# Optimization experiments

Hardware: AMD Instinct MI355X
Metric: run time of the kernel (lower is better)

Reference implementation:

```python
import jax, jax.numpy as jnp
import numpy as np

BETA = 0.99
EPS = 1e-05


def setup_inputs() -> dict:
    key = jax.random.key(0)
    s = jax.random.normal(key, (16, 2000, 257, 2), dtype=jnp.float32)
    return {"s": s}


def reference(s):
    # s: (N, T, F, C). Unbiased EWMA mean/var normalization, sequential over T.
    N, T, F, C = s.shape
    st = jnp.transpose(s, (1, 0, 2, 3))  # (T, N, F, C) for scan over time
    zeros = jnp.zeros((N, F, C), dtype=s.dtype)
    one = jnp.asarray(1.0, dtype=s.dtype)
    beta = jnp.asarray(BETA, dtype=s.dtype)

    def step(carry, x):
        beta_t, v1, v2, S = carry
        beta_t = beta * beta_t
        v1 = beta * v1 + (1 - beta) * x
        v2_prev = v2
        v2 = v1 / (1 - beta_t)
        w = (1 - beta) / (1 - beta_t)
        S = (1 - w) * S + w * (x - v2) * (x - v2_prev)
        S = S * (S > 0)  # clamp negative variance to 0 (as in original)
        y = (x - v2) / jnp.sqrt(S + EPS)
        return (beta_t, v1, v2, S), y

    init = (one, zeros, zeros, zeros)
    _, out = jax.lax.scan(step, init, st)
    return jnp.transpose(out, (1, 0, 2, 3))  # back to (N, T, F, C)
```

## Files before the change

### kernel.cpp

```cpp
#include <hip/hip_runtime.h>


#define NN 16
#define TT 2000
#define FCC 514
#define SERIES (NN * FCC)
#define BETAF 0.99f
#define OMBF 0.01f
#define EPSF 1e-5f
#define NCHUNK 7
#define CLEN 286
#define WARM 512
#define PF 16

__global__ __launch_bounds__(64)
void ewma_kernel(const float* __restrict__ s, float* __restrict__ out) {
    const int tid = blockIdx.x * 64 + threadIdx.x;
    if (tid >= SERIES) return;

    const int chunk = blockIdx.y;
    const int t_out = chunk * CLEN;
    int t_end = t_out + CLEN; if (t_end > TT) t_end = TT;
    int t0 = t_out - WARM;     if (t0 < 0) t0 = 0;

    const int n  = tid / FCC;
    const int fc = tid - n * FCC;

    double bd = 0.99, acc = 1.0;
    int e = t0;
    while (e) { if (e & 1) acc *= bd; bd *= bd; e >>= 1; }
    float bt = (float)acc;

    float v1 = 0.0f, v2p = 0.0f, S = 0.0f;

    const size_t base = (size_t)n * TT * FCC + (size_t)fc + (size_t)t0 * FCC;
    const float* p  = s   + base;
    float*       po = out + base;

    auto step = [&](float x) -> float {
        bt *= BETAF;
        const float om = 1.0f - bt;
        const float r  = __builtin_amdgcn_rcpf(om);
        v1 = fmaf(BETAF, v1 - x, x);
        const float v2 = v1 * r;
        const float w  = OMBF * r;
        const float d  = x - v2;
        const float dp = x - v2p;
        const float pr = d * dp;
        S = fmaf(w, pr - S, S);
        S = fmaxf(S, 0.0f);
        const float y = d * __builtin_amdgcn_rsqf(S + EPSF);
        v2p = v2;
        return y;
    };

    float buf[PF];
    #pragma unroll
    for (int i = 0; i < PF; ++i) buf[i] = p[i * FCC];

    int t = t0;
    while (t + PF <= t_end) {
        const float* pf_ptr = (t + 2 * PF <= t_end) ? (p + PF * FCC) : p;
        float nbuf[PF];
        #pragma unroll
        for (int i = 0; i < PF; ++i) nbuf[i] = pf_ptr[i * FCC];

        #pragma unroll
        for (int i = 0; i < PF; ++i) {
            const float y = step(buf[i]);
            if (t >= t_out) {
                po[i * FCC] = y;
            } else if (t + i >= t_out) {
                po[i * FCC] = y;
            }
        }

        #pragma unroll
        for (int i = 0; i < PF; ++i) buf[i] = nbuf[i];
        p  += PF * FCC;
        po += PF * FCC;
        t  += PF;
    }
    for (; t < t_end; ++t) {
        const float y = step(*p);
        if (t >= t_out) *po = y;
        p  += FCC;
        po += FCC;
    }
}

extern "C" void kernel_launch(void* const* d_in, const int* in_sizes, int n_in,
                              void* d_out, int out_size, void* d_ws, size_t ws_size,
                              hipStream_t stream) {
    const float* s = (const float*)d_in[0];
    float* out = (float*)d_out;
    dim3 grid((SERIES + 63) / 64, NCHUNK);
    ewma_kernel<<<grid, dim3(64), 0, stream>>>(s, out);
}
```

Measured before the change: 154.7 us.

## Precompute bias-correction table in LDS and split time into more chunks

```diff
diff --git a/kernel.cpp b/kernel.cpp
--- a/kernel.cpp
+++ b/kernel.cpp
@@ -8,28 +8,38 @@
 #define BETAF 0.99f
 #define OMBF 0.01f
 #define EPSF 1e-5f
-#define NCHUNK 7
-#define CLEN 286
+#define NCHUNK 16
+#define CLEN 125
 #define WARM 512
 #define PF 16
+#define TABMAX (WARM + CLEN)
 
 __global__ __launch_bounds__(64)
 void ewma_kernel(const float* __restrict__ s, float* __restrict__ out) {
-    const int tid = blockIdx.x * 64 + threadIdx.x;
-    if (tid >= SERIES) return;
+    __shared__ float2 tab[TABMAX];
 
     const int chunk = blockIdx.y;
     const int t_out = chunk * CLEN;
     int t_end = t_out + CLEN; if (t_end > TT) t_end = TT;
     int t0 = t_out - WARM;     if (t0 < 0) t0 = 0;
+    const int L = t_end - t0;
+
+    for (int i = threadIdx.x; i < L; i += 64) {
+        double bd = 0.99, acc = 1.0;
+        int e = t0 + i + 1;
+        #pragma unroll
+        for (int k = 0; k < 11; ++k) { if (e & 1) acc *= bd; bd *= bd; e >>= 1; }
+        const float om = 1.0f - (float)acc;
+        const float r  = __builtin_amdgcn_rcpf(om);
+        tab[i] = make_float2(r, OMBF * r);
+    }
+    __syncthreads();
+
+    const int tid = blockIdx.x * 64 + threadIdx.x;
+    if (tid >= SERIES) return;
 
     const int n  = tid / FCC;
     const int fc = tid - n * FCC;
-
-    double bd = 0.99, acc = 1.0;
-    int e = t0;
-    while (e) { if (e & 1) acc *= bd; bd *= bd; e >>= 1; }
-    float bt = (float)acc;
 
     float v1 = 0.0f, v2p = 0.0f, S = 0.0f;
 
@@ -37,17 +47,14 @@
     const float* p  = s   + base;
     float*       po = out + base;
 
-    auto step = [&](float x) -> float {
-        bt *= BETAF;
-        const float om = 1.0f - bt;
-        const float r  = __builtin_amdgcn_rcpf(om);
-        v1 = fmaf(BETAF, v1 - x, x);
-        const float v2 = v1 * r;
-        const float w  = OMBF * r;
-        const float d  = x - v2;
-        const float dp = x - v2p;
-        const float pr = d * dp;
-        S = fmaf(w, pr - S, S);
+    auto step = [&](float x, float2 rw) -> float {
+        const float r = rw.x, w = rw.y;
+        v1 = fmaf(BETAF, v1, OMBF * x);
+        const float v2  = v1 * r;
+        const float d   = x - v2;
+        const float dp  = x - v2p;
+        const float wpr = w * (d * dp);
+        S = fmaf(S, 1.0f - w, wpr);
         S = fmaxf(S, 0.0f);
         const float y = d * __builtin_amdgcn_rsqf(S + EPSF);
         v2p = v2;
@@ -59,6 +66,7 @@
     for (int i = 0; i < PF; ++i) buf[i] = p[i * FCC];
 
     int t = t0;
+    int li = 0;
     while (t + PF <= t_end) {
         const float* pf_ptr = (t + 2 * PF <= t_end) ? (p + PF * FCC) : p;
         float nbuf[PF];
@@ -67,7 +75,7 @@
 
         #pragma unroll
         for (int i = 0; i < PF; ++i) {
-            const float y = step(buf[i]);
+            const float y = step(buf[i], tab[li + i]);
             if (t >= t_out) {
                 po[i * FCC] = y;
             } else if (t + i >= t_out) {
@@ -80,9 +88,10 @@
         p  += PF * FCC;
         po += PF * FCC;
         t  += PF;
+        li += PF;
     }
-    for (; t < t_end; ++t) {
-        const float y = step(*p);
+    for (; t < t_end; ++t, ++li) {
+        const float y = step(*p, tab[li]);
         if (t >= t_out) *po = y;
         p  += FCC;
         po += FCC;
```

Measured after the change: 165.2 us. +6.8%, slower.

## Stage input through LDS with async global_load_lds triple buffering per batch row

Applied to the files above, without the earlier changes.

```diff
diff --git a/kernel.cpp b/kernel.cpp
--- a/kernel.cpp
+++ b/kernel.cpp
@@ -4,89 +4,220 @@
 #define NN 16
 #define TT 2000
 #define FCC 514
-#define SERIES (NN * FCC)
+#define BPT 2056
 #define BETAF 0.99f
 #define OMBF 0.01f
 #define EPSF 1e-5f
 #define NCHUNK 7
 #define CLEN 286
 #define WARM 512
-#define PF 16
-
-__global__ __launch_bounds__(64)
+#define G 16
+#define GRPB (G * BPT)
+#define SLOTB 36864
+#define NSLOT 3
+
+__device__ __constant__ const float BP[G + 1] = {
+    1.0f, 0.99f, 0.9801f, 0.970299f, 0.96059601f, 0.9509900499f,
+    0.941480149401f, 0.93206534790699f, 0.9227446944279201f,
+    0.9134272474836409f, 0.9042929750088045f, 0.8952500452587165f,
+    0.8862975448061293f, 0.877434569357868f, 0.8686602236642894f,
+    0.8599736214276465f, 0.8513738852133700f
+};
+
+#define READX                                                                \
+    float x[G];                                                              \
+    {                                                                        \
+        unsigned a = ldsbase + (unsigned)((g % NSLOT) * SLOTB) + d           \
+                   + (unsigned)fc * 4u;                                      \
+        _Pragma("unroll")                                                    \
+        for (int i = 0; i < G; ++i) {                                        \
+            asm volatile("ds_read_b32 %0, %1" : "=v"(x[i]) : "v"(a));        \
+            a += BPT;                                                        \
+        }                                                                    \
+        asm volatile("s_waitcnt lgkmcnt(0)" ::: "memory");                   \
+        __builtin_amdgcn_sched_barrier(0);                                   \
+    }
+
+#define RCPB                                                                 \
+    float rr[G];                                                             \
+    _Pragma("unroll")                                                        \
+    for (int i = 0; i < G; ++i)                                              \
+        rr[i] = __builtin_amdgcn_rcpf(1.0f - btg * BP[i]);                   \
+    btg *= BP[G];
+
+#define KEEP16(Y)                                                            \
+    asm volatile("" :: "v"(Y[0]), "v"(Y[1]), "v"(Y[2]), "v"(Y[3]),           \
+                       "v"(Y[4]), "v"(Y[5]), "v"(Y[6]), "v"(Y[7]),           \
+                       "v"(Y[8]), "v"(Y[9]), "v"(Y[10]), "v"(Y[11]),         \
+                       "v"(Y[12]), "v"(Y[13]), "v"(Y[14]), "v"(Y[15]));
+
+#define BODY_OUT(Y)                                                          \
+    {                                                                        \
+        READX                                                                \
+        STAGE(g + 2);                                                        \
+        RCPB                                                                 \
+        float* pg = Ofp + (size_t)t * FCC + fc;                              \
+        _Pragma("unroll")                                                    \
+        for (int i = 0; i < G; ++i) {                                        \
+            const float xx = x[i];                                           \
+            const float r  = rr[i];                                          \
+            v1 = fmaf(BETAF, v1, OMBF * xx);                                 \
+            const float v2 = v1 * r;                                         \
+            const float dd = xx - v2;                                        \
+            const float dp = xx - v2p;                                       \
+            S = fmaf(OMBF * r, dd * dp - S, S);                              \
+            S = fmaxf(S, 0.0f);                                              \
+            Y[i] = dd * __builtin_amdgcn_rsqf(S + EPSF);                     \
+            v2p = v2;                                                        \
+            if (fc < FCC)                                                    \
+                asm volatile("global_store_dword %0, %1, off"                \
+                             :: "v"(pg + i * FCC), "v"(Y[i]));               \
+        }                                                                    \
+            \
+        asm volatile("s_waitcnt vmcnt(20)" ::: "memory");                    \
+        __builtin_amdgcn_sched_barrier(0);                                   \
+        KEEP16(yA) KEEP16(yB)                                                \
+        __builtin_amdgcn_s_barrier();                                        \
+    }
+
+__global__ __launch_bounds__(576, 1)
 void ewma_kernel(const float* __restrict__ s, float* __restrict__ out) {
-    const int tid = blockIdx.x * 64 + threadIdx.x;
-    if (tid >= SERIES) return;
-
+    __shared__ char lds[NSLOT * SLOTB];
+
+    const int lane = threadIdx.x & 63;
+    const int wid  = threadIdx.x >> 6;
+    const int fc   = threadIdx.x;
+    const int n    = blockIdx.x;
     const int chunk = blockIdx.y;
+
     const int t_out = chunk * CLEN;
     int t_end = t_out + CLEN; if (t_end > TT) t_end = TT;
     int t0 = t_out - WARM;     if (t0 < 0) t0 = 0;
 
-    const int n  = tid / FCC;
-    const int fc = tid - n * FCC;
-
-    double bd = 0.99, acc = 1.0;
-    int e = t0;
-    while (e) { if (e & 1) acc *= bd; bd *= bd; e >>= 1; }
-    float bt = (float)acc;
+    const char* Bn     = (const char*)s + (size_t)n * TT * BPT;
+    const char* send16 = (const char*)s + (size_t)NN * TT * BPT - 16;
+    const unsigned d   = (unsigned)((t0 & 1) * 8);
+
+    const unsigned ldsbase =
+        (unsigned)(uintptr_t)(__attribute__((address_space(3))) char*)lds;
+
+    const char* Astage0 = Bn + (size_t)t0 * BPT - d;
+
+    auto STAGE = [&](int k) {
+        const char* A = Astage0 + (size_t)k * GRPB;
+        char* slot = lds + (k % NSLOT) * SLOTB;
+        #pragma unroll
+        for (int j = 0; j < 4; ++j) {
+            const int o = wid * 4 + j;
+            const char* src = A + o * 1024 + lane * 16;
+            if (src > send16) src = send16;
+            __builtin_amdgcn_global_load_lds(
+                (const __attribute__((address_space(1))) void*)src,
+                (__attribute__((address_space(3))) void*)(slot + o * 1024),
+                16, 0, 0);
+        }
+    };
+
+    float btg;
+    {
+        double bd = 0.99, acc = 0.99;
+        int e = t0;
+        while (e) { if (e & 1) acc *= bd; bd *= bd; e >>= 1; }
+        btg = (float)acc;
+    }
 
     float v1 = 0.0f, v2p = 0.0f, S = 0.0f;
-
-    const size_t base = (size_t)n * TT * FCC + (size_t)fc + (size_t)t0 * FCC;
-    const float* p  = s   + base;
-    float*       po = out + base;
-
-    auto step = [&](float x) -> float {
-        bt *= BETAF;
-        const float om = 1.0f - bt;
-        const float r  = __builtin_amdgcn_rcpf(om);
-        v1 = fmaf(BETAF, v1 - x, x);
-        const float v2 = v1 * r;
-        const float w  = OMBF * r;
-        const float d  = x - v2;
-        const float dp = x - v2p;
-        const float pr = d * dp;
-        S = fmaf(w, pr - S, S);
-        S = fmaxf(S, 0.0f);
-        const float y = d * __builtin_amdgcn_rsqf(S + EPSF);
-        v2p = v2;
-        return y;
-    };
-
-    float buf[PF];
+    float* Ofp = out + (size_t)n * TT * FCC;
+
+    STAGE(0); STAGE(1);
+    asm volatile("s_waitcnt vmcnt(4)" ::: "memory");
+    __builtin_amdgcn_sched_barrier(0);
+    __builtin_amdgcn_s_barrier();
+
+    int t = t0, g = 0;
+
+    while (t + G <= t_out) {
+        READX
+        STAGE(g + 2);
+        RCPB
+        #pragma unroll
+        for (int i = 0; i < G; ++i) {
+            const float xx = x[i];
+            const float r  = rr[i];
+            v1 = fmaf(BETAF, v1, OMBF * xx);
+            const float v2 = v1 * r;
+            const float dd = xx - v2;
+            const float dp = xx - v2p;
+            S = fmaf(OMBF * r, dd * dp - S, S);
+            S = fmaxf(S, 0.0f);
+            v2p = v2;
+        }
+        asm volatile("s_waitcnt vmcnt(4)" ::: "memory");
+        __builtin_amdgcn_sched_barrier(0);
+        __builtin_amdgcn_s_barrier();
+        ++g; t += G;
+    }
+
+    if (t < t_out && t + G <= t_end) {
+        READX
+        STAGE(g + 2);
+        RCPB
+        float* pg = Ofp + (size_t)t * FCC + fc;
+        #pragma unroll
+        for (int i = 0; i < G; ++i) {
+            const float xx = x[i];
+            const float r  = rr[i];
+            v1 = fmaf(BETAF, v1, OMBF * xx);
+            const float v2 = v1 * r;
+            const float dd = xx - v2;
+            const float dp = xx - v2p;
+            S = fmaf(OMBF * r, dd * dp - S, S);
+            S = fmaxf(S, 0.0f);
+            const float y = dd * __builtin_amdgcn_rsqf(S + EPSF);
+            v2p = v2;
+            if (t + i >= t_out && fc < FCC)
+                asm volatile("global_store_dword %0, %1, off"
+                             :: "v"(pg + i * FCC), "v"(y));
+        }
+        asm volatile("s_waitcnt vmcnt(0)" ::: "memory");
+        __builtin_amdgcn_sched_barrier(0);
+        __builtin_amdgcn_s_barrier();
+        ++g; t += G;
+    }
+
+    float yA[G], yB[G];
     #pragma unroll
-    for (int i = 0; i < PF; ++i) buf[i] = p[i * FCC];
-
-    int t = t0;
-    while (t + PF <= t_end) {
-        const float* pf_ptr = (t + 2 * PF <= t_end) ? (p + PF * FCC) : p;
-        float nbuf[PF];
-        #pragma unroll
-        for (int i = 0; i < PF; ++i) nbuf[i] = pf_ptr[i * FCC];
-
-        #pragma unroll
-        for (int i = 0; i < PF; ++i) {
-            const float y = step(buf[i]);
-            if (t >= t_out) {
-                po[i * FCC] = y;
-            } else if (t + i >= t_out) {
-                po[i * FCC] = y;
-            }
-        }
-
-        #pragma unroll
-        for (int i = 0; i < PF; ++i) buf[i] = nbuf[i];
-        p  += PF * FCC;
-        po += PF * FCC;
-        t  += PF;
-    }
-    for (; t < t_end; ++t) {
-        const float y = step(*p);
-        if (t >= t_out) *po = y;
-        p  += FCC;
-        po += FCC;
-    }
+    for (int i = 0; i < G; ++i) { yA[i] = 0.0f; yB[i] = 0.0f; }
+    int cur = 0;
+    while (t + G <= t_end) {
+        if (cur == 0) BODY_OUT(yA)
+        else          BODY_OUT(yB)
+        cur ^= 1;
+        ++g; t += G;
+    }
+
+    {
+        const int R = t_end - t;
+        const float* slotf = (const float*)(lds + (g % NSLOT) * SLOTB);
+        const unsigned d4 = d >> 2;
+        for (int i = 0; i < R; ++i) {
+            const float xx = slotf[d4 + i * FCC + fc];
+            const float r  = __builtin_amdgcn_rcpf(1.0f - btg);
+            btg *= BETAF;
+            v1 = fmaf(BETAF, v1, OMBF * xx);
+            const float v2 = v1 * r;
+            const float dd = xx - v2;
+            const float dp = xx - v2p;
+            S = fmaf(OMBF * r, dd * dp - S, S);
+            S = fmaxf(S, 0.0f);
+            const float y = dd * __builtin_amdgcn_rsqf(S + EPSF);
+            v2p = v2;
+            if (t + i >= t_out && fc < FCC)
+                Ofp[(size_t)(t + i) * FCC + fc] = y;
+        }
+    }
+
+    asm volatile("s_waitcnt vmcnt(0)" ::: "memory");
 }
 
 extern "C" void kernel_launch(void* const* d_in, const int* in_sizes, int n_in,
@@ -94,6 +225,6 @@
                               hipStream_t stream) {
     const float* s = (const float*)d_in[0];
     float* out = (float*)d_out;
-    dim3 grid((SERIES + 63) / 64, NCHUNK);
-    ewma_kernel<<<grid, dim3(64), 0, stream>>>(s, out);
+    dim3 grid(NN, NCHUNK);
+    ewma_kernel<<<grid, dim3(576), 0, stream>>>(s, out);
 }
```

New measurement: 174.2 us. 1.13x slower.
